# Optimization experiments

Measured on AMD Instinct MI355X. Metric: run time of the kernel, lower is better.

## Reference

```python
import jax, jax.numpy as jnp
import numpy as np

LATENT, HID, STYLE, S = 16, 256, 64, 10
B = 16384

def _lin_init(key, fan_in, shape):
    # torch nn.Linear default: U(-1/sqrt(fan_in), 1/sqrt(fan_in))
    bound = 1.0 / np.sqrt(fan_in)
    return jax.random.uniform(key, shape, jnp.float32, -bound, bound)

def setup_inputs() -> dict:
    key = jax.random.key(0)
    ks = jax.random.split(key, 32)
    inp = {
        "z": jax.random.normal(ks[0], (B, LATENT), jnp.float32),
        "y": jax.random.randint(ks[1], (B,), 0, S),
        # shared 4-layer MLP
        "sw0": _lin_init(ks[2], LATENT, (LATENT, HID)), "sb0": _lin_init(ks[3], LATENT, (HID,)),
        "sw1": _lin_init(ks[4], HID, (HID, HID)), "sb1": _lin_init(ks[5], HID, (HID,)),
        "sw2": _lin_init(ks[6], HID, (HID, HID)), "sb2": _lin_init(ks[7], HID, (HID,)),
        "sw3": _lin_init(ks[8], HID, (HID, HID)), "sb3": _lin_init(ks[9], HID, (HID,)),
        # unshared per-speaker branches, stacked over speaker axis
        "uw0": _lin_init(ks[10], HID, (S, HID, HID)), "ub0": _lin_init(ks[11], HID, (S, HID)),
        "uw1": _lin_init(ks[12], HID, (S, HID, HID)), "ub1": _lin_init(ks[13], HID, (S, HID)),
        "uw2": _lin_init(ks[14], HID, (S, HID, HID)), "ub2": _lin_init(ks[15], HID, (S, HID)),
        "uw3": _lin_init(ks[16], HID, (S, HID, STYLE)), "ub3": _lin_init(ks[17], HID, (S, STYLE)),
    }
    return inp

def reference(z, y, sw0, sb0, sw1, sb1, sw2, sb2, sw3, sb3,
              uw0, ub0, uw1, ub1, uw2, ub2, uw3, ub3):
    relu = jax.nn.relu
    # shared trunk: [B, HID]
    h = relu(z @ sw0 + sb0)
    h = relu(h @ sw1 + sb1)
    h = relu(h @ sw2 + sb2)
    h = relu(h @ sw3 + sb3)
    # all speaker branches computed for every sample (faithful to original)
    t = relu(jnp.einsum('bh,shk->bsk', h, uw0) + ub0)  # [B, S, HID]
    t = relu(jnp.einsum('bsh,shk->bsk', t, uw1) + ub1)
    t = relu(jnp.einsum('bsh,shk->bsk', t, uw2) + ub2)
    out = jnp.einsum('bsh,shk->bsk', t, uw3) + ub3      # [B, S, STYLE]
    # gather branch by speaker id
    s = out[jnp.arange(out.shape[0]), y]                # [B, STYLE]
    return s
```

## Files before the change

### kernel.cpp

```cpp
#include <hip/hip_runtime.h>

#define B_TOT 16384
#define LAT   16
#define HID   256
#define STY   64
#define NS    10
#define RB    16
#define RBM   32
#define PAD   20
#define NBK   64

#define WS_CNT   0
#define WS_SEG   16
#define WS_BLK   32
#define WS_BCNT  64
#define WS_IDX   (WS_BCNT + NBK*NS)
#define IDX_CAP  (B_TOT + NS*64)
#define WS_INTS  (WS_IDX + IDX_CAP)
#define WGT_OFF_EL (((WS_INTS*4 + 255)/256)*128 + 384)
#define TOT_WEL  2334720
#define N_CHUNK  4560

typedef __attribute__((ext_vector_type(8))) short bf16x8;
typedef __attribute__((ext_vector_type(4))) float f32x4;
typedef unsigned long long ull;

static __device__ __forceinline__ ushort f2bf(float x) {
    union { float f; unsigned u; } c; c.f = x;
    unsigned u = c.u;
    unsigned r = u + 0x7FFFu + ((u >> 16) & 1u);
    return (ushort)(r >> 16);
}

__global__ __launch_bounds__(256) void k_blkhist(const int* __restrict__ y, int* __restrict__ ws) {
    __shared__ int h[NS];
    int t = threadIdx.x;
    if (t < NS) h[t] = 0;
    __syncthreads();
    atomicAdd(&h[y[blockIdx.x * 256 + t]], 1);
    __syncthreads();
    if (t < NS) ws[WS_BCNT + blockIdx.x * NS + t] = h[t];
}

__global__ __launch_bounds__(256) void k_prep2(const int* __restrict__ y, int* __restrict__ ws, int rb) {
    __shared__ int tot_sh[NS], excl_sh[NS], off_sh[NS];
    const int t = threadIdx.x, wv = t >> 6, l = t & 63;
    const int myb = blockIdx.x;

    for (int s = wv; s < NS; s += 4) {
        int c = ws[WS_BCNT + l * NS + s];
        int inc = c;
        #pragma unroll
        for (int o = 1; o < 64; o <<= 1) {
            int v = __shfl_up(inc, o, 64);
            if (l >= o) inc += v;
        }
        int tot = __shfl(inc, 63, 64);
        int exc = __shfl(inc, myb, 64) - __shfl(c, myb, 64);
        if (l == 0) { tot_sh[s] = tot; excl_sh[s] = exc; }
    }
    __syncthreads();
    if (t < NS) {
        int ab = 0, ae = 0;
        for (int q = 0; q < t; ++q) {
            int cq = tot_sh[q];
            int nb = (cq + rb - 1) / rb;
            ab += nb; ae += nb * rb;
        }
        off_sh[t] = ae + excl_sh[t];
        if (myb == 0) {
            ws[WS_CNT + t] = tot_sh[t];
            ws[WS_SEG + t] = ae;
            ws[WS_BLK + t] = ab;
        }
    }
    if (myb == 0 && t == 0) {
        int ab = 0;
        for (int q = 0; q < NS; ++q) ab += (tot_sh[q] + rb - 1) / rb;
        ws[WS_BLK + NS] = ab;
    }
    __syncthreads();
    int b = myb * 256 + t;
    int p = atomicAdd(&off_sh[y[b]], 1);
    ws[WS_IDX + p] = b;
}

__global__ __launch_bounds__(256) void k_conv(
    const float* __restrict__ sw0, const float* __restrict__ sw1,
    const float* __restrict__ sw2, const float* __restrict__ sw3,
    const float* __restrict__ uw0, const float* __restrict__ uw1,
    const float* __restrict__ uw2, const float* __restrict__ uw3,
    ushort* __restrict__ wgt,
    const int* __restrict__ y, int* __restrict__ ws)
{
    __shared__ float tile[4][32][18];
    __shared__ int h[NS];

    if (blockIdx.x < NBK) {
        int t = threadIdx.x;
        if (t < NS) h[t] = 0;
        __syncthreads();
        atomicAdd(&h[y[blockIdx.x * 256 + t]], 1);
        __syncthreads();
        if (t < NS) ws[WS_BCNT + blockIdx.x * NS + t] = h[t];
    }

    int wid = blockIdx.x * 4 + (threadIdx.x >> 6);
    int wv  = threadIdx.x >> 6;
    int l   = threadIdx.x & 63;
    int lc  = l & 15, lh = l >> 4;

    const float* src; int Ksrc, N, kb, nt;
    if (wid < 16) {
        src = sw0; Ksrc = LAT; N = 256; kb = 0; nt = wid;
    } else if (wid < 400) {
        int c = wid - 16; int ly = c >> 7; int r = c & 127;
        src = (ly == 0 ? sw1 : ly == 1 ? sw2 : sw3);
        Ksrc = 256; N = 256; kb = r >> 4; nt = r & 15;
    } else {
        int c = wid - 400; int s = c / 416; int r = c % 416;
        if (r < 384) {
            int ly = r >> 7; int rr = r & 127;
            src = (ly == 0 ? uw0 : ly == 1 ? uw1 : uw2) + (long)s * 65536;
            Ksrc = 256; N = 256; kb = rr >> 4; nt = rr & 15;
        } else {
            int rr = r - 384;
            src = uw3 + (long)s * 16384;
            Ksrc = 256; N = STY; kb = rr >> 2; nt = rr & 3;
        }
    }

    #pragma unroll
    for (int it = 0; it < 2; ++it) {
        int r = it * 16 + (l >> 2);
        int k = kb * 32 + r;
        float4 v = make_float4(0.f, 0.f, 0.f, 0.f);
        if (k < Ksrc) v = *(const float4*)(src + (long)k * N + nt * 16 + (l & 3) * 4);
        int c = (l & 3) * 4;
        tile[wv][r][c] = v.x; tile[wv][r][c + 1] = v.y;
        tile[wv][r][c + 2] = v.z; tile[wv][r][c + 3] = v.w;
    }
    __syncthreads();

    ushort v[8];
    #pragma unroll
    for (int j = 0; j < 8; ++j) v[j] = f2bf(tile[wv][lh * 8 + j][lc]);
    uint4 o;
    o.x = (unsigned)v[0] | ((unsigned)v[1] << 16);
    o.y = (unsigned)v[2] | ((unsigned)v[3] << 16);
    o.z = (unsigned)v[4] | ((unsigned)v[5] << 16);
    o.w = (unsigned)v[6] | ((unsigned)v[7] << 16);
    *(uint4*)(wgt + (long)wid * 512 + l * 8) = o;
}

__global__ __launch_bounds__(512, 4) void k_main_bf(
    const float* __restrict__ z, const int* __restrict__ y,
    const int* __restrict__ ws, const ushort* __restrict__ wgt,
    const float* __restrict__ sb0, const float* __restrict__ sb1,
    const float* __restrict__ sb2, const float* __restrict__ sb3,
    const float* __restrict__ ub0, const float* __restrict__ ub1,
    const float* __restrict__ ub2, const float* __restrict__ ub3,
    float* __restrict__ out)
{
    int bid = blockIdx.x;
    {
        int nwg = gridDim.x, q8 = nwg >> 3, r8 = nwg & 7;
        int x = bid & 7, p = bid >> 3;
        bid = (x < r8 ? x * (q8 + 1) : r8 * (q8 + 1) + (x - r8) * q8) + p;
    }

    __shared__ ushort act[2][32][RBM][8];
    __shared__ ull pk[65][3];
    __shared__ int bidx[RBM];

    const int t = threadIdx.x, w = t >> 6, l = t & 63;
    const int lc = l & 15, lh = l >> 4;
    const int nt0 = w * 2;

    if (w == 0) {
        const int* cb = ws + WS_BCNT + l * NS;
        ull a0 = (ull)cb[0] | ((ull)cb[1] << 16) | ((ull)cb[2] << 32) | ((ull)cb[3] << 48);
        ull a1 = (ull)cb[4] | ((ull)cb[5] << 16) | ((ull)cb[6] << 32) | ((ull)cb[7] << 48);
        ull a2 = (ull)cb[8] | ((ull)cb[9] << 16);
        ull s0 = a0, s1 = a1, s2 = a2;
        #pragma unroll
        for (int o = 1; o < 64; o <<= 1) {
            ull v0 = __shfl_up(s0, o, 64);
            ull v1 = __shfl_up(s1, o, 64);
            ull v2 = __shfl_up(s2, o, 64);
            if (l >= o) { s0 += v0; s1 += v1; s2 += v2; }
        }
        pk[l][0] = s0 - a0; pk[l][1] = s1 - a1; pk[l][2] = s2 - a2;
        if (l == 63) { pk[64][0] = s0; pk[64][1] = s1; pk[64][2] = s2; }
    }
    __syncthreads();

    const ull g0 = pk[64][0], g1 = pk[64][1], g2 = pk[64][2];
    #define TOTQ(q_) ((int)((((q_) < 4) ? g0 : (((q_) < 8) ? g1 : g2)) >> (((q_) & 3) * 16)) & 0xFFFF)
    int s = -1, loc = 0, cnt = 0;
    {
        int ab = 0;
        #pragma unroll
        for (int q = 0; q < NS; ++q) {
            int tq = TOTQ(q);
            int nb = (tq + RBM - 1) >> 5;
            if (s < 0 && bid < ab + nb) { s = q; loc = bid - ab; cnt = tq; }
            ab += nb;
        }
    }
    #undef TOTQ
    if (s < 0) return;
    int nval = cnt - loc * RBM;
    if (nval > RBM) nval = RBM;
    const int lo = loc * RBM, hi = lo + RBM;
    const int sh = (s & 3) * 16;

    #pragma unroll
    for (int bo = 0; bo < 8; ++bo) {
        int b = w * 8 + bo;
        ull pbp = (s < 4) ? pk[b][0]     : ((s < 8) ? pk[b][1]     : pk[b][2]);
        ull pnp = (s < 4) ? pk[b + 1][0] : ((s < 8) ? pk[b + 1][1] : pk[b + 1][2]);
        int Pb = (int)((pbp >> sh) & 0xFFFF);
        int Pn = (int)((pnp >> sh) & 0xFFFF);
        if (Pb < hi && Pn > lo) {
            int4 v = *(const int4*)(y + b * 256 + l * 4);
            int m0 = (v.x == s), m1 = (v.y == s), m2 = (v.z == s), m3 = (v.w == s);
            int c = m0 + m1 + m2 + m3;
            int inc = c;
            #pragma unroll
            for (int o = 1; o < 64; o <<= 1) {
                int u = __shfl_up(inc, o, 64);
                if (l >= o) inc += u;
            }
            int r  = Pb + inc - c;
            int gi = b * 256 + l * 4;
            if (m0) { if (r >= lo && r < hi) bidx[r - lo] = gi;     ++r; }
            if (m1) { if (r >= lo && r < hi) bidx[r - lo] = gi + 1; ++r; }
            if (m2) { if (r >= lo && r < hi) bidx[r - lo] = gi + 2; ++r; }
            if (m3) { if (r >= lo && r < hi) bidx[r - lo] = gi + 3; ++r; }
        }
    }
    __syncthreads();

    if (t < RBM * 4) {
        int row = t >> 2, q = t & 3;
        int gb  = (row < nval) ? bidx[row] : 0;
        float4 zv = *(const float4*)(z + (long)gb * LAT + q * 4);
        ushort4 pv; pv.x = f2bf(zv.x); pv.y = f2bf(zv.y); pv.z = f2bf(zv.z); pv.w = f2bf(zv.w);
        *(ushort4*)&act[0][q >> 1][row][(q & 1) * 4] = pv;
        ushort4 zr; zr.x = zr.y = zr.z = zr.w = 0;
        *(ushort4*)&act[0][2 + (q >> 1)][row][(q & 1) * 4] = zr;
    }
    __syncthreads();

    {
        f32x4 acc[2][2];
        #pragma unroll
        for (int q = 0; q < 2; ++q) {
            float4 bv = *(const float4*)(sb0 + (nt0 + q) * 16 + lh * 4);
            #pragma unroll
            for (int rt = 0; rt < 2; ++rt) acc[q][rt] = (f32x4){bv.x, bv.y, bv.z, bv.w};
        }
        bf16x8 Wf[2];
        #pragma unroll
        for (int q = 0; q < 2; ++q)
            Wf[q] = *(const bf16x8*)(wgt + ((nt0 + q) * 64 + l) * 8);
        #pragma unroll
        for (int rt = 0; rt < 2; ++rt) {
            bf16x8 av = *(const bf16x8*)&act[0][lh][rt * 16 + lc][0];
            #pragma unroll
            for (int q = 0; q < 2; ++q)
                acc[q][rt] = __builtin_amdgcn_mfma_f32_16x16x32_bf16(Wf[q], av, acc[q][rt], 0, 0, 0);
        }
        #pragma unroll
        for (int q = 0; q < 2; ++q) {
            int n0 = (nt0 + q) * 16 + lh * 4;
            #pragma unroll
            for (int rt = 0; rt < 2; ++rt) {
                ushort4 u;
                u.x = f2bf(fmaxf(acc[q][rt][0], 0.f));
                u.y = f2bf(fmaxf(acc[q][rt][1], 0.f));
                u.z = f2bf(fmaxf(acc[q][rt][2], 0.f));
                u.w = f2bf(fmaxf(acc[q][rt][3], 0.f));
                *(ushort4*)&act[1][n0 >> 3][rt * 16 + lc][n0 & 7] = u;
            }
        }
    }
    __syncthreads();

    auto midlayer = [&](const ushort* __restrict__ wf, const float* __restrict__ bs, int src) {
        const int dst = src ^ 1;
        f32x4 acc[2][2];
        #pragma unroll
        for (int q = 0; q < 2; ++q) {
            float4 bv = *(const float4*)(bs + (nt0 + q) * 16 + lh * 4);
            #pragma unroll
            for (int rt = 0; rt < 2; ++rt) acc[q][rt] = (f32x4){bv.x, bv.y, bv.z, bv.w};
        }
        bf16x8 Bc[2], Bn[2];
        #pragma unroll
        for (int q = 0; q < 2; ++q)
            Bc[q] = *(const bf16x8*)(wf + ((nt0 + q) * 64 + l) * 8);
        #pragma unroll
        for (int kb = 0; kb < 8; ++kb) {
            if (kb < 7) {
                #pragma unroll
                for (int q = 0; q < 2; ++q)
                    Bn[q] = *(const bf16x8*)(wf + (((kb + 1) * 16 + nt0 + q) * 64 + l) * 8);
            }
            #pragma unroll
            for (int rt = 0; rt < 2; ++rt) {
                bf16x8 av = *(const bf16x8*)&act[src][kb * 4 + lh][rt * 16 + lc][0];
                #pragma unroll
                for (int q = 0; q < 2; ++q)
                    acc[q][rt] = __builtin_amdgcn_mfma_f32_16x16x32_bf16(Bc[q], av, acc[q][rt], 0, 0, 0);
            }
            #pragma unroll
            for (int q = 0; q < 2; ++q) Bc[q] = Bn[q];
        }
        #pragma unroll
        for (int q = 0; q < 2; ++q) {
            int n0 = (nt0 + q) * 16 + lh * 4;
            #pragma unroll
            for (int rt = 0; rt < 2; ++rt) {
                ushort4 u;
                u.x = f2bf(fmaxf(acc[q][rt][0], 0.f));
                u.y = f2bf(fmaxf(acc[q][rt][1], 0.f));
                u.z = f2bf(fmaxf(acc[q][rt][2], 0.f));
                u.w = f2bf(fmaxf(acc[q][rt][3], 0.f));
                *(ushort4*)&act[dst][n0 >> 3][rt * 16 + lc][n0 & 7] = u;
            }
        }
        __syncthreads();
    };

    midlayer(wgt + 8192,   sb1, 1);
    midlayer(wgt + 73728,  sb2, 0);
    midlayer(wgt + 139264, sb3, 1);
    const long sbse = 204800 + (long)s * 212992;
    midlayer(wgt + sbse,          ub0 + s * HID, 0);
    midlayer(wgt + sbse + 65536,  ub1 + s * HID, 1);
    midlayer(wgt + sbse + 131072, ub2 + s * HID, 0);

    {
        const ushort* wf = wgt + sbse + 196608;
        const float*  bs = ub3 + s * STY;
        const int nt = w & 3, rt = w >> 2;
        const int n0 = nt * 16 + lh * 4;
        f32x4 acc;
        {
            float4 bv = *(const float4*)(bs + n0);
            acc = (f32x4){bv.x, bv.y, bv.z, bv.w};
        }
        bf16x8 Bc = *(const bf16x8*)(wf + (nt * 64 + l) * 8);
        bf16x8 Bn;
        #pragma unroll
        for (int kb = 0; kb < 8; ++kb) {
            if (kb < 7) Bn = *(const bf16x8*)(wf + (((kb + 1) * 4 + nt) * 64 + l) * 8);
            bf16x8 av = *(const bf16x8*)&act[1][kb * 4 + lh][rt * 16 + lc][0];
            acc = __builtin_amdgcn_mfma_f32_16x16x32_bf16(Bc, av, acc, 0, 0, 0);
            Bc = Bn;
        }
        int row = rt * 16 + lc;
        if (row < nval) {
            int gb = bidx[row];
            float4 o = make_float4(acc[0], acc[1], acc[2], acc[3]);
            *(float4*)(out + (long)gb * STY + n0) = o;
        }
    }
}

#define FMA16(wv_, hv_) do { \
    acc[0][0] = fmaf(hv_.x, wv_.x, acc[0][0]); \
    acc[0][1] = fmaf(hv_.y, wv_.x, acc[0][1]); \
    acc[0][2] = fmaf(hv_.z, wv_.x, acc[0][2]); \
    acc[0][3] = fmaf(hv_.w, wv_.x, acc[0][3]); \
    acc[1][0] = fmaf(hv_.x, wv_.y, acc[1][0]); \
    acc[1][1] = fmaf(hv_.y, wv_.y, acc[1][1]); \
    acc[1][2] = fmaf(hv_.z, wv_.y, acc[1][2]); \
    acc[1][3] = fmaf(hv_.w, wv_.y, acc[1][3]); \
    acc[2][0] = fmaf(hv_.x, wv_.z, acc[2][0]); \
    acc[2][1] = fmaf(hv_.y, wv_.z, acc[2][1]); \
    acc[2][2] = fmaf(hv_.z, wv_.z, acc[2][2]); \
    acc[2][3] = fmaf(hv_.w, wv_.z, acc[2][3]); \
    acc[3][0] = fmaf(hv_.x, wv_.w, acc[3][0]); \
    acc[3][1] = fmaf(hv_.y, wv_.w, acc[3][1]); \
    acc[3][2] = fmaf(hv_.z, wv_.w, acc[3][2]); \
    acc[3][3] = fmaf(hv_.w, wv_.w, acc[3][3]); \
} while (0)

__global__ __launch_bounds__(256, 3) void k_main_f32(
    const float* __restrict__ z,
    const int* __restrict__ ws,
    const float* __restrict__ sw0, const float* __restrict__ sb0,
    const float* __restrict__ sw1, const float* __restrict__ sb1,
    const float* __restrict__ sw2, const float* __restrict__ sb2,
    const float* __restrict__ sw3, const float* __restrict__ sb3,
    const float* __restrict__ uw0, const float* __restrict__ ub0,
    const float* __restrict__ uw1, const float* __restrict__ ub1,
    const float* __restrict__ uw2, const float* __restrict__ ub2,
    const float* __restrict__ uw3, const float* __restrict__ ub3,
    float* __restrict__ out)
{
    const int bid = blockIdx.x;
    if (bid >= ws[WS_BLK + NS]) return;
    int s = 0;
    #pragma unroll
    for (int q = 0; q < NS - 1; ++q)
        if (bid >= ws[WS_BLK + q + 1]) s = q + 1;
    const int loc  = bid - ws[WS_BLK + s];
    int nval = ws[WS_CNT + s] - loc * RB;
    if (nval > RB) nval = RB;
    const int base = ws[WS_SEG + s] + loc * RB;

    __shared__ int bidx[RB];
    __shared__ __align__(16) float zt[LAT][PAD];
    __shared__ __align__(16) float ht[2][HID][PAD];

    const int t = threadIdx.x;
    if (t < RB) {
        int gb = ws[WS_IDX + base + t];
        bidx[t] = (t < nval) ? gb : 0;
    }
    __syncthreads();
    { int r = t & (RB - 1), k = t >> 4; zt[k][r] = z[bidx[r] * LAT + k]; }
    __syncthreads();

    const int cg = t & 63, wvi = t >> 6, c0 = cg * 4, r0 = wvi * 4;
    float acc[4][4];
    {
        float4 bv = *(const float4*)(sb0 + c0);
        #pragma unroll
        for (int ri = 0; ri < 4; ++ri) { acc[0][ri] = bv.x; acc[1][ri] = bv.y; acc[2][ri] = bv.z; acc[3][ri] = bv.w; }
        #pragma unroll
        for (int k = 0; k < LAT; ++k) {
            float4 wv = *(const float4*)(sw0 + k * HID + c0);
            float4 hv = *(const float4*)(&zt[k][r0]);
            FMA16(wv, hv);
        }
        #pragma unroll
        for (int ci = 0; ci < 4; ++ci) {
            float4 v;
            v.x = fmaxf(acc[ci][0], 0.f); v.y = fmaxf(acc[ci][1], 0.f);
            v.z = fmaxf(acc[ci][2], 0.f); v.w = fmaxf(acc[ci][3], 0.f);
            *(float4*)&ht[0][c0 + ci][r0] = v;
        }
    }
    __syncthreads();

    auto midlayer = [&](const float* __restrict__ W, const float* __restrict__ bs, int src) {
        float4 bv = *(const float4*)(bs + c0);
        #pragma unroll
        for (int ri = 0; ri < 4; ++ri) { acc[0][ri] = bv.x; acc[1][ri] = bv.y; acc[2][ri] = bv.z; acc[3][ri] = bv.w; }
        #pragma unroll 4
        for (int k = 0; k < HID; ++k) {
            float4 wv = *(const float4*)(W + k * HID + c0);
            float4 hv = *(const float4*)(&ht[src][k][r0]);
            FMA16(wv, hv);
        }
        const int dst = src ^ 1;
        #pragma unroll
        for (int ci = 0; ci < 4; ++ci) {
            float4 v;
            v.x = fmaxf(acc[ci][0], 0.f); v.y = fmaxf(acc[ci][1], 0.f);
            v.z = fmaxf(acc[ci][2], 0.f); v.w = fmaxf(acc[ci][3], 0.f);
            *(float4*)&ht[dst][c0 + ci][r0] = v;
        }
    };

    midlayer(sw1, sb1, 0); __syncthreads();
    midlayer(sw2, sb2, 1); __syncthreads();
    midlayer(sw3, sb3, 0); __syncthreads();
    const long so = (long)s;
    midlayer(uw0 + so * HID * HID, ub0 + so * HID, 1); __syncthreads();
    midlayer(uw1 + so * HID * HID, ub1 + so * HID, 0); __syncthreads();
    midlayer(uw2 + so * HID * HID, ub2 + so * HID, 1); __syncthreads();

    {
        const float* W  = uw3 + so * HID * STY;
        const float* bs = ub3 + so * STY;
        const int c64 = (t & 15) * 4, rr = t >> 4;
        float4 bv = *(const float4*)(bs + c64);
        float a0 = bv.x, a1 = bv.y, a2 = bv.z, a3 = bv.w;
        #pragma unroll 4
        for (int k = 0; k < HID; ++k) {
            float4 wv = *(const float4*)(W + k * STY + c64);
            float  hv = ht[0][k][rr];
            a0 = fmaf(hv, wv.x, a0); a1 = fmaf(hv, wv.y, a1);
            a2 = fmaf(hv, wv.z, a2); a3 = fmaf(hv, wv.w, a3);
        }
        if (rr < nval) *(float4*)(out + (long)bidx[rr] * STY + c64) = make_float4(a0, a1, a2, a3);
    }
}

extern "C" void kernel_launch(void* const* d_in, const int* in_sizes, int n_in,
                              void* d_out, int out_size, void* d_ws, size_t ws_size,
                              hipStream_t stream) {
    const float* z   = (const float*)d_in[0];
    const int*   y   = (const int*)  d_in[1];
    const float* sw0 = (const float*)d_in[2];  const float* sb0 = (const float*)d_in[3];
    const float* sw1 = (const float*)d_in[4];  const float* sb1 = (const float*)d_in[5];
    const float* sw2 = (const float*)d_in[6];  const float* sb2 = (const float*)d_in[7];
    const float* sw3 = (const float*)d_in[8];  const float* sb3 = (const float*)d_in[9];
    const float* uw0 = (const float*)d_in[10]; const float* ub0 = (const float*)d_in[11];
    const float* uw1 = (const float*)d_in[12]; const float* ub1 = (const float*)d_in[13];
    const float* uw2 = (const float*)d_in[14]; const float* ub2 = (const float*)d_in[15];
    const float* uw3 = (const float*)d_in[16]; const float* ub3 = (const float*)d_in[17];
    float* out = (float*)d_out;
    int*   ws  = (int*)d_ws;

    const size_t req = (size_t)WGT_OFF_EL * 2 + (size_t)TOT_WEL * 2;
    const bool bfp = (ws_size >= req);

    if (bfp) {
        ushort* wgt = (ushort*)d_ws + WGT_OFF_EL;
        k_conv<<<N_CHUNK / 4, 256, 0, stream>>>(sw0, sw1, sw2, sw3, uw0, uw1, uw2, uw3, wgt, y, ws);
        const int nblocks = B_TOT / RBM + NS;
        k_main_bf<<<nblocks, 512, 0, stream>>>(z, y, ws, wgt,
            sb0, sb1, sb2, sb3, ub0, ub1, ub2, ub3, out);
    } else {
        k_blkhist<<<NBK, 256, 0, stream>>>(y, ws);
        k_prep2  <<<NBK, 256, 0, stream>>>(y, ws, RB);
        const int nblocks = B_TOT / RB + NS;
        k_main_f32<<<nblocks, 256, 0, stream>>>(z, ws,
            sw0, sb0, sw1, sb1, sw2, sb2, sw3, sb3,
            uw0, ub0, uw1, ub1, uw2, ub2, uw3, ub3, out);
    }
}
```

Baseline: 40.15 us.

## Double row block to 64 and remap waves to one column tile each

```diff
diff --git a/kernel.cpp b/kernel.cpp
--- a/kernel.cpp
+++ b/kernel.cpp
@@ -6,7 +6,7 @@
 #define STY   64
 #define NS    10
 #define RB    16
-#define RBM   32
+#define RBM   64
 #define PAD   20
 #define NBK   64
 
@@ -153,7 +153,7 @@
     *(uint4*)(wgt + (long)wid * 512 + l * 8) = o;
 }
 
-__global__ __launch_bounds__(512, 4) void k_main_bf(
+__global__ __launch_bounds__(1024, 4) void k_main_bf(
     const float* __restrict__ z, const int* __restrict__ y,
     const int* __restrict__ ws, const ushort* __restrict__ wgt,
     const float* __restrict__ sb0, const float* __restrict__ sb1,
@@ -175,7 +175,6 @@
 
     const int t = threadIdx.x, w = t >> 6, l = t & 63;
     const int lc = l & 15, lh = l >> 4;
-    const int nt0 = w * 2;
 
     if (w == 0) {
         const int* cb = ws + WS_BCNT + l * NS;
@@ -203,7 +202,7 @@
         #pragma unroll
         for (int q = 0; q < NS; ++q) {
             int tq = TOTQ(q);
-            int nb = (tq + RBM - 1) >> 5;
+            int nb = (tq + RBM - 1) >> 6;
             if (s < 0 && bid < ab + nb) { s = q; loc = bid - ab; cnt = tq; }
             ab += nb;
         }
@@ -216,8 +215,8 @@
     const int sh = (s & 3) * 16;
 
     #pragma unroll
-    for (int bo = 0; bo < 8; ++bo) {
-        int b = w * 8 + bo;
+    for (int bo = 0; bo < 4; ++bo) {
+        int b = w * 4 + bo;
         ull pbp = (s < 4) ? pk[b][0]     : ((s < 8) ? pk[b][1]     : pk[b][2]);
         ull pnp = (s < 4) ? pk[b + 1][0] : ((s < 8) ? pk[b + 1][1] : pk[b + 1][2]);
         int Pb = (int)((pbp >> sh) & 0xFFFF);
@@ -254,82 +253,61 @@
     __syncthreads();
 
     {
-        f32x4 acc[2][2];
-        #pragma unroll
-        for (int q = 0; q < 2; ++q) {
-            float4 bv = *(const float4*)(sb0 + (nt0 + q) * 16 + lh * 4);
+        f32x4 acc[4];
+        const int n0 = w * 16 + lh * 4;
+        {
+            float4 bv = *(const float4*)(sb0 + n0);
             #pragma unroll
-            for (int rt = 0; rt < 2; ++rt) acc[q][rt] = (f32x4){bv.x, bv.y, bv.z, bv.w};
-        }
-        bf16x8 Wf[2];
-        #pragma unroll
-        for (int q = 0; q < 2; ++q)
-            Wf[q] = *(const bf16x8*)(wgt + ((nt0 + q) * 64 + l) * 8);
-        #pragma unroll
-        for (int rt = 0; rt < 2; ++rt) {
+            for (int rt = 0; rt < 4; ++rt) acc[rt] = (f32x4){bv.x, bv.y, bv.z, bv.w};
+        }
+        bf16x8 Wf = *(const bf16x8*)(wgt + (w * 64 + l) * 8);
+        #pragma unroll
+        for (int rt = 0; rt < 4; ++rt) {
             bf16x8 av = *(const bf16x8*)&act[0][lh][rt * 16 + lc][0];
-            #pragma unroll
-            for (int q = 0; q < 2; ++q)
-                acc[q][rt] = __builtin_amdgcn_mfma_f32_16x16x32_bf16(Wf[q], av, acc[q][rt], 0, 0, 0);
-        }
-        #pragma unroll
-        for (int q = 0; q < 2; ++q) {
-            int n0 = (nt0 + q) * 16 + lh * 4;
-            #pragma unroll
-            for (int rt = 0; rt < 2; ++rt) {
-                ushort4 u;
-                u.x = f2bf(fmaxf(acc[q][rt][0], 0.f));
-                u.y = f2bf(fmaxf(acc[q][rt][1], 0.f));
-                u.z = f2bf(fmaxf(acc[q][rt][2], 0.f));
-                u.w = f2bf(fmaxf(acc[q][rt][3], 0.f));
-                *(ushort4*)&act[1][n0 >> 3][rt * 16 + lc][n0 & 7] = u;
-            }
+            acc[rt] = __builtin_amdgcn_mfma_f32_16x16x32_bf16(Wf, av, acc[rt], 0, 0, 0);
+        }
+        #pragma unroll
+        for (int rt = 0; rt < 4; ++rt) {
+            ushort4 u;
+            u.x = f2bf(fmaxf(acc[rt][0], 0.f));
+            u.y = f2bf(fmaxf(acc[rt][1], 0.f));
+            u.z = f2bf(fmaxf(acc[rt][2], 0.f));
+            u.w = f2bf(fmaxf(acc[rt][3], 0.f));
+            *(ushort4*)&act[1][n0 >> 3][rt * 16 + lc][n0 & 7] = u;
         }
     }
     __syncthreads();
 
     auto midlayer = [&](const ushort* __restrict__ wf, const float* __restrict__ bs, int src) {
         const int dst = src ^ 1;
-        f32x4 acc[2][2];
-        #pragma unroll
-        for (int q = 0; q < 2; ++q) {
-            float4 bv = *(const float4*)(bs + (nt0 + q) * 16 + lh * 4);
+        const int n0 = w * 16 + lh * 4;
+        f32x4 acc[4];
+        {
+            float4 bv = *(const float4*)(bs + n0);
             #pragma unroll
-            for (int rt = 0; rt < 2; ++rt) acc[q][rt] = (f32x4){bv.x, bv.y, bv.z, bv.w};
-        }
-        bf16x8 Bc[2], Bn[2];
-        #pragma unroll
-        for (int q = 0; q < 2; ++q)
-            Bc[q] = *(const bf16x8*)(wf + ((nt0 + q) * 64 + l) * 8);
+            for (int rt = 0; rt < 4; ++rt) acc[rt] = (f32x4){bv.x, bv.y, bv.z, bv.w};
+        }
+        bf16x8 Bc = *(const bf16x8*)(wf + (w * 64 + l) * 8);
+        bf16x8 Bn;
         #pragma unroll
         for (int kb = 0; kb < 8; ++kb) {
-            if (kb < 7) {
-                #pragma unroll
-                for (int q = 0; q < 2; ++q)
-                    Bn[q] = *(const bf16x8*)(wf + (((kb + 1) * 16 + nt0 + q) * 64 + l) * 8);
+            if (kb < 7)
+                Bn = *(const bf16x8*)(wf + (((kb + 1) * 16 + w) * 64 + l) * 8);
+            #pragma unroll
+            for (int rt = 0; rt < 4; ++rt) {
+                bf16x8 av = *(const bf16x8*)&act[src][kb * 4 + lh][rt * 16 + lc][0];
+                acc[rt] = __builtin_amdgcn_mfma_f32_16x16x32_bf16(Bc, av, acc[rt], 0, 0, 0);
             }
-            #pragma unroll
-            for (int rt = 0; rt < 2; ++rt) {
-                bf16x8 av = *(const bf16x8*)&act[src][kb * 4 + lh][rt * 16 + lc][0];
-                #pragma unroll
-                for (int q = 0; q < 2; ++q)
-                    acc[q][rt] = __builtin_amdgcn_mfma_f32_16x16x32_bf16(Bc[q], av, acc[q][rt], 0, 0, 0);
-            }
-            #pragma unroll
-            for (int q = 0; q < 2; ++q) Bc[q] = Bn[q];
-        }
-        #pragma unroll
-        for (int q = 0; q < 2; ++q) {
-            int n0 = (nt0 + q) * 16 + lh * 4;
-            #pragma unroll
-            for (int rt = 0; rt < 2; ++rt) {
-                ushort4 u;
-                u.x = f2bf(fmaxf(acc[q][rt][0], 0.f));
-                u.y = f2bf(fmaxf(acc[q][rt][1], 0.f));
-                u.z = f2bf(fmaxf(acc[q][rt][2], 0.f));
-                u.w = f2bf(fmaxf(acc[q][rt][3], 0.f));
-                *(ushort4*)&act[dst][n0 >> 3][rt * 16 + lc][n0 & 7] = u;
-            }
+            Bc = Bn;
+        }
+        #pragma unroll
+        for (int rt = 0; rt < 4; ++rt) {
+            ushort4 u;
+            u.x = f2bf(fmaxf(acc[rt][0], 0.f));
+            u.y = f2bf(fmaxf(acc[rt][1], 0.f));
+            u.z = f2bf(fmaxf(acc[rt][2], 0.f));
+            u.w = f2bf(fmaxf(acc[rt][3], 0.f));
+            *(ushort4*)&act[dst][n0 >> 3][rt * 16 + lc][n0 & 7] = u;
         }
         __syncthreads();
     };
@@ -516,7 +494,7 @@
         ushort* wgt = (ushort*)d_ws + WGT_OFF_EL;
         k_conv<<<N_CHUNK / 4, 256, 0, stream>>>(sw0, sw1, sw2, sw3, uw0, uw1, uw2, uw3, wgt, y, ws);
         const int nblocks = B_TOT / RBM + NS;
-        k_main_bf<<<nblocks, 512, 0, stream>>>(z, y, ws, wgt,
+        k_main_bf<<<nblocks, 1024, 0, stream>>>(z, y, ws, wgt,
             sb0, sb1, sb2, sb3, ub0, ub1, ub2, ub3, out);
     } else {
         k_blkhist<<<NBK, 256, 0, stream>>>(y, ws);
```

Measured after the change: 39.71 us. Within noise of the previous version (-1.1%).
